# Kernel tuning notes

Hardware: AMD Instinct MI355X
Metric: run time of the kernel (lower is better)

## Reference

```python
import jax, jax.numpy as jnp
import numpy as np

B, S, D, H = 2, 2048, 1024, 16
DK = D // H  # 64
THETA = 10000.0


def setup_inputs() -> dict:
    key = jax.random.key(0)
    ks = jax.random.split(key, 5)
    std = float(np.sqrt(2.0 / (D + D)))
    x = jax.random.normal(ks[0], (B, S, D), dtype=jnp.float32)
    q_proj = jax.random.normal(ks[1], (D, D), dtype=jnp.float32) * std
    k_proj = jax.random.normal(ks[2], (D, D), dtype=jnp.float32) * std
    v_proj = jax.random.normal(ks[3], (D, D), dtype=jnp.float32) * std
    o_proj = jax.random.normal(ks[4], (D, D), dtype=jnp.float32) * std
    token_positions = jnp.arange(S, dtype=jnp.int32).reshape(1, S)
    return {"x": x, "token_positions": token_positions,
            "q_proj": q_proj, "k_proj": k_proj, "v_proj": v_proj, "o_proj": o_proj}


def _rope(t, pos):
    # t: [B, H, S, DK]; pos: [S]. Equivalent to multiplying by the block-diagonal
    # rotation matrix R[pos] in the source (interleaved 2x2 rotations).
    inv_freq = 1.0 / (THETA ** (2.0 * jnp.arange(DK // 2, dtype=jnp.float32) / DK))
    ang = pos.astype(jnp.float32)[:, None] * inv_freq[None, :]  # [S, DK/2]
    c, s = jnp.cos(ang), jnp.sin(ang)
    t0, t1 = t[..., 0::2], t[..., 1::2]
    out0 = c * t0 - s * t1
    out1 = s * t0 + c * t1
    return jnp.stack([out0, out1], axis=-1).reshape(t.shape)


def reference(x, token_positions, q_proj, k_proj, v_proj, o_proj):
    def split_heads(t):  # [B,S,D] -> [B,H,S,DK]
        return t.reshape(B, S, H, DK).transpose(0, 2, 1, 3)

    q = split_heads(jnp.einsum('bsd,ed->bse', x, q_proj))
    k = split_heads(jnp.einsum('bsd,ed->bse', x, k_proj))
    v = split_heads(jnp.einsum('bsd,ed->bse', x, v_proj))

    pos = token_positions[0]
    q = _rope(q, pos)
    k = _rope(k, pos)

    scores = jnp.einsum('bhqd,bhkd->bhqk', q, k) / jnp.sqrt(jnp.float32(DK))
    causal = jnp.tril(jnp.ones((S, S), dtype=bool))
    scores = jnp.where(causal, scores, -jnp.inf)

    # Faithful to source softmax: subtract the GLOBAL max (x.max()), then row-normalize.
    p = jnp.exp(scores - jnp.max(scores))
    p = p / jnp.sum(p, axis=-1, keepdims=True)

    attn = jnp.einsum('bhqk,bhkd->bhqd', p, v)
    attn = attn.transpose(0, 2, 1, 3).reshape(B, S, D)  # merge heads
    return jnp.einsum('bsd,ed->bse', attn, o_proj)
```

## Files before the change

### kernel.cpp

```cpp
#include <hip/hip_runtime.h>
#include <math.h>

#define B_  2
#define S_  2048
#define D_  1024
#define H_  16
#define DK_ 64
#define M_  (B_ * S_)

using u16 = unsigned short;
using u32 = unsigned int;
typedef __attribute__((ext_vector_type(8))) short  short8;
typedef __attribute__((ext_vector_type(4))) short  short4v;
typedef __attribute__((ext_vector_type(4))) float  float4v;
typedef __attribute__((ext_vector_type(4))) float  f32x4;
typedef __attribute__((ext_vector_type(4))) u32    u32x4;

__device__ __forceinline__ float bf2f(u16 h) {
  u32 u = ((u32)h) << 16;
  return __builtin_bit_cast(float, u);
}
__device__ __forceinline__ u16 f2bf(float f) {
  u32 u = __builtin_bit_cast(u32, f);
  u32 r = u + 0x7fffu + ((u >> 16) & 1u);
  return (u16)(r >> 16);
}

__device__ __forceinline__ void async16(const void* g, void* l) {
  __builtin_amdgcn_global_load_lds((const __attribute__((address_space(1))) void*)g,
                                   (__attribute__((address_space(3))) void*)l,
                                   16, 0, 0);
}

#define MFMA16(a, b, c) __builtin_amdgcn_mfma_f32_16x16x32_bf16((a), (b), (c), 0, 0, 0)

__device__ __forceinline__ void stc(u16* p, float v)   { *p = f2bf(v); }
__device__ __forceinline__ void stc(float* p, float v) { *p = v; }

#define XG_ (M_ * D_ / 4)
#define WG_ (D_ * D_ / 4)
__global__ __launch_bounds__(256) void cvt5_kernel(
    const float* __restrict__ x,  const float* __restrict__ wq,
    const float* __restrict__ wk, const float* __restrict__ wv,
    const float* __restrict__ wo, u16* __restrict__ Xb, u16* __restrict__ Wqb,
    u16* __restrict__ Wkb, u16* __restrict__ Wvb, u16* __restrict__ Wob) {
  int i = blockIdx.x * 256 + threadIdx.x;
  const float* s; u16* d; int off;
  if (i < XG_)                { s = x;  d = Xb;  off = i; }
  else if (i < XG_ + WG_)     { s = wq; d = Wqb; off = i - XG_; }
  else if (i < XG_ + 2 * WG_) { s = wk; d = Wkb; off = i - XG_ - WG_; }
  else if (i < XG_ + 3 * WG_) { s = wv; d = Wvb; off = i - XG_ - 2 * WG_; }
  else                        { s = wo; d = Wob; off = i - XG_ - 3 * WG_; }
  f32x4 v = ((const f32x4*)s)[off];
  short4v o;
  o[0] = (short)f2bf(v[0]); o[1] = (short)f2bf(v[1]);
  o[2] = (short)f2bf(v[2]); o[3] = (short)f2bf(v[3]);
  ((short4v*)d)[off] = o;
}

template <typename TC>
__device__ __forceinline__ void gemm_tile(const u16* __restrict__ A,
                                          const u16* __restrict__ Bw,
                                          TC* __restrict__ C,
                                          int K, int N, int m0, int n0) {
  __shared__ __align__(16) u16 As[128 * 32];
  __shared__ __align__(16) u16 Bs[128 * 32];
  const int tid  = threadIdx.x;
  const int lane = tid & 63;
  const int wave = tid >> 6;
  const int quad = lane >> 4;
  const int l15  = lane & 15;
  const int wm   = (wave >> 1) << 6;
  const int wn   = (wave & 1) << 6;

  float4v acc[4][4];
#pragma unroll
  for (int i = 0; i < 4; ++i)
#pragma unroll
    for (int j = 0; j < 4; ++j) acc[i][j] = (float4v){0.f, 0.f, 0.f, 0.f};

  for (int k0 = 0; k0 < K; k0 += 32) {
#pragma unroll
    for (int i = 0; i < 2; ++i) {
      const int cbase = i * 256 + wave * 64;
      const int c     = cbase + lane;
      async16(A  + (size_t)(m0 + (c >> 2)) * K + k0 + ((c & 3) << 3), As + cbase * 8);
      async16(Bw + (size_t)(n0 + (c >> 2)) * K + k0 + ((c & 3) << 3), Bs + cbase * 8);
    }
    __syncthreads();

    short8 af[4], bfr[4];
#pragma unroll
    for (int mi = 0; mi < 4; ++mi)
      af[mi] = *(const short8*)(As + (wm + mi * 16 + l15) * 32 + quad * 8);
#pragma unroll
    for (int ni = 0; ni < 4; ++ni)
      bfr[ni] = *(const short8*)(Bs + (wn + ni * 16 + l15) * 32 + quad * 8);
#pragma unroll
    for (int mi = 0; mi < 4; ++mi)
#pragma unroll
      for (int ni = 0; ni < 4; ++ni)
        acc[mi][ni] = MFMA16(af[mi], bfr[ni], acc[mi][ni]);
    __syncthreads();
  }

#pragma unroll
  for (int mi = 0; mi < 4; ++mi)
#pragma unroll
    for (int ni = 0; ni < 4; ++ni)
#pragma unroll
      for (int r = 0; r < 4; ++r) {
        const int row = m0 + wm + mi * 16 + quad * 4 + r;
        const int col = n0 + wn + ni * 16 + l15;
        stc(C + (size_t)row * N + col, acc[mi][ni][r]);
      }
}

__global__ __launch_bounds__(256) void gemm_qkv_kernel(
    const u16* __restrict__ X, const u16* __restrict__ Wq,
    const u16* __restrict__ Wk, const u16* __restrict__ Wv,
    u16* Qb, u16* Kb, u16* Vb) {
  const int mt  = blockIdx.x;
  const int nn  = blockIdx.y;
  const int sel = nn >> 3;
  const int nt  = nn & 7;
  const u16* Bw = (sel == 0) ? Wq : (sel == 1) ? Wk : Wv;
  u16*       C  = (sel == 0) ? Qb : (sel == 1) ? Kb : Vb;
  gemm_tile(X, Bw, C, D_, D_, mt * 128, nt * 128);
}

__global__ __launch_bounds__(256) void gemm_o_kernel(
    const u16* __restrict__ Ab, const u16* __restrict__ Wo, float* Out) {
  gemm_tile(Ab, Wo, Out, D_, D_, blockIdx.x * 128, blockIdx.y * 128);
}

__global__ __launch_bounds__(256) void rv_kernel(u16* __restrict__ Qb,
                                                 u16* __restrict__ Kb,
                                                 const void* __restrict__ posv,
                                                 const u16* __restrict__ Vb,
                                                 u16* __restrict__ Vt) {
  __shared__ float tabc[2][32], tabs[2][32];
  __shared__ __align__(16) u16 T[64 * 72];
  const int tid = threadIdx.x;

  if (blockIdx.x < 2048) {
    const int bx = blockIdx.x;
    const int t  = bx * 256 + tid;
    const int p4 = t & 7;
    const int h  = (t >> 3) & (H_ - 1);
    const int s  = (t >> 7) & (S_ - 1);
    const int b  = t >> 18;
    const int* p32 = (const int*)posv;
    const bool is64 = (p32[1] == 0 && p32[2] == 1);
    if (tid < 64) {
      const int sl = tid >> 5, i = tid & 31;
      const int sg = ((bx * 2) & (S_ - 1)) + sl;
      const int ps = is64 ? p32[2 * sg] : p32[sg];
      const float freq = exp2f(-0.4152410118609203f * (float)i);
      float sn, cs;
      sincosf((float)ps * freq, &sn, &cs);
      tabc[sl][i] = cs; tabs[sl][i] = sn;
    }
    __syncthreads();
    const int sl = (tid >> 7) & 1;
    const size_t base = (size_t)(b * S_ + s) * D_ + h * DK_ + p4 * 8;
    short8 qv = *(const short8*)(Qb + base);
    short8 kv = *(const short8*)(Kb + base);
    short8 qo, ko;
#pragma unroll
    for (int j = 0; j < 4; ++j) {
      const int i = p4 * 4 + j;
      const float cs = tabc[sl][i], sn = tabs[sl][i];
      const float q0v = bf2f((u16)qv[2 * j]), q1v = bf2f((u16)qv[2 * j + 1]);
      qo[2 * j]     = (short)f2bf(0.125f * (cs * q0v - sn * q1v));
      qo[2 * j + 1] = (short)f2bf(0.125f * (sn * q0v + cs * q1v));
      const float k0v = bf2f((u16)kv[2 * j]), k1v = bf2f((u16)kv[2 * j + 1]);
      ko[2 * j]     = (short)f2bf(cs * k0v - sn * k1v);
      ko[2 * j + 1] = (short)f2bf(sn * k0v + cs * k1v);
    }
    *(short8*)(Qb + base) = qo;
    *(short8*)(Kb + base) = ko;
  } else {
    const int idx  = blockIdx.x - 2048;
    const int sblk = idx & 31;
    const int bh   = idx >> 5;
    const int b = bh >> 4, h = bh & 15;
    const int s0 = sblk * 64;
    {
      const int srow = tid >> 2;
      const int dseg = (tid & 3) << 4;
      const u16* g = Vb + (size_t)(b * S_ + s0 + srow) * D_ + h * DK_ + dseg;
      *(short8*)(T + srow * 72 + dseg)     = *(const short8*)(g);
      *(short8*)(T + srow * 72 + dseg + 8) = *(const short8*)(g + 8);
    }
    __syncthreads();
    {
      const int dk   = tid >> 2;
      const int sseg = (tid & 3) << 4;
      short8 o0, o1;
#pragma unroll
      for (int jj = 0; jj < 8; ++jj) {
        const int ss0 = sseg + jj;
        const int ss1 = sseg + 8 + jj;
        const int k0l = (((ss0 & 31) >> 3) << 2) + (((ss0 >> 2) & 1) << 4) +
                        (ss0 & 3) + (ss0 & 32);
        const int k1l = (((ss1 & 31) >> 3) << 2) + (((ss1 >> 2) & 1) << 4) +
                        (ss1 & 3) + (ss1 & 32);
        o0[jj] = (short)T[k0l * 72 + dk];
        o1[jj] = (short)T[k1l * 72 + dk];
      }
      u16* g = Vt + (size_t)(bh * DK_ + dk) * S_ + s0 + sseg;
      *(short8*)(g)     = o0;
      *(short8*)(g + 8) = o1;
    }
  }
}

__global__ __launch_bounds__(256, 4) void attn_kernel(const u16* __restrict__ Qb,
                                                      const u16* __restrict__ Kb,
                                                      const u16* __restrict__ Vt,
                                                      u16* __restrict__ Ob) {
  const int j5 = (blockIdx.x + blockIdx.y) & 31;
  const int r5 = j5 & 7, g5 = j5 >> 3;
  const int qt = (g5 == 0) ? r5 : (g5 == 1) ? r5 + 8 : (g5 == 2) ? 23 - r5 : 31 - r5;
  const int bh = blockIdx.y;
  const int b = bh >> 4, h = bh & 15;
  const int tid = threadIdx.x, lane = tid & 63, wave = tid >> 6;
  const int qh = wave >> 1, kh = wave & 1;
  const int quad = lane >> 4, l15 = lane & 15;
  const int qw = qt * 64 + qh * 32;

  __shared__ __align__(16) u16 SM[2][2][64 * 64];

  const char* kp = (const char*)(Kb + (size_t)b * S_ * D_ + h * DK_);
  const char* vp = (const char*)(Vt + (size_t)bh * DK_ * S_);

  int koffb[2], voffb[2];
#pragma unroll
  for (int i = 0; i < 2; ++i) {
    const int c  = wave * 128 + i * 64 + lane;
    const int kr = c >> 3;
    const int kj = (c & 7) ^ (kr & 7);
    koffb[i] = kr * (D_ * 2) + kj * 16;
    const int vdk = c >> 3;
    const int vj  = (c & 7) ^ (vdk & 7);
    voffb[i] = vdk * (S_ * 2) + vj * 16;
  }

  auto stage = [&](int sel) {
#pragma unroll
    for (int i = 0; i < 2; ++i) {
      const int cb = wave * 128 + i * 64;
      async16(kp + koffb[i], &SM[0][sel][cb * 8]);
      async16(vp + voffb[i], &SM[1][sel][cb * 8]);
    }
    kp += 64 * D_ * 2;
    vp += 128;
  };

  const int x7   = l15 & 7;
  const int krd0 = (kh * 32 + l15) * 64 + ((quad ^ x7) << 3);
  const int krd1 = (kh * 32 + l15) * 64 + (((quad + 4) ^ x7) << 3);
  const int vrd  = l15 * 64 + (((kh * 4 + quad) ^ x7) << 3);

  short8 qf[2][2];
#pragma unroll
  for (int rg = 0; rg < 2; ++rg) {
    const u16* qrow = Qb + (size_t)(b * S_ + qw + rg * 16 + l15) * D_ + h * DK_;
    qf[rg][0] = *(const short8*)(qrow + quad * 8);
    qf[rg][1] = *(const short8*)(qrow + 32 + quad * 8);
  }

  short8 ones;
#pragma unroll
  for (int j = 0; j < 8; ++j) ones[j] = (short)0x3F80;

  float4v oacc[2][4];
#pragma unroll
  for (int rg = 0; rg < 2; ++rg)
#pragma unroll
    for (int n2 = 0; n2 < 4; ++n2) oacc[rg][n2] = (float4v){0.f, 0.f, 0.f, 0.f};
  float4v lacc[2] = {(float4v){0.f, 0.f, 0.f, 0.f}, (float4v){0.f, 0.f, 0.f, 0.f}};

  const int NS = qt + 1;
  stage(0);

  for (int j = 0; j < NS; ++j) {
    asm volatile("s_waitcnt vmcnt(0)" ::: "memory");
    __builtin_amdgcn_s_barrier();
    asm volatile("" ::: "memory");
    if (j + 1 < NS) stage((j + 1) & 1);

    const u16* ks = &SM[0][j & 1][0];
    const u16* vs = &SM[1][j & 1][0];

    float4v sc[2][2];
    __builtin_amdgcn_s_setprio(1);
#pragma unroll
    for (int ni = 0; ni < 2; ++ni) {
      const short8 kf0 = *(const short8*)(ks + krd0 + ni * 1024);
      const short8 kf1 = *(const short8*)(ks + krd1 + ni * 1024);
      float4v z = (float4v){0.f, 0.f, 0.f, 0.f};
      sc[0][ni] = MFMA16(kf1, qf[0][1], MFMA16(kf0, qf[0][0], z));
      sc[1][ni] = MFMA16(kf1, qf[1][1], MFMA16(kf0, qf[1][0], z));
    }
    __builtin_amdgcn_s_setprio(0);

    const int kb = j * 64 + kh * 32;
    if (kb + 31 > qw) {
#pragma unroll
      for (int rg = 0; rg < 2; ++rg) {
        const int qr = qw + rg * 16 + l15;
#pragma unroll
        for (int ni = 0; ni < 2; ++ni)
#pragma unroll
          for (int r = 0; r < 4; ++r) {
            const float e = __expf(sc[rg][ni][r]);
            sc[rg][ni][r] = (kb + ni * 16 + quad * 4 + r > qr) ? 0.f : e;
          }
      }
    } else {
#pragma unroll
      for (int rg = 0; rg < 2; ++rg)
#pragma unroll
        for (int ni = 0; ni < 2; ++ni)
#pragma unroll
          for (int r = 0; r < 4; ++r) sc[rg][ni][r] = __expf(sc[rg][ni][r]);
    }

    short8 pfr[2];
#pragma unroll
    for (int rg = 0; rg < 2; ++rg) {
      u32 w0, w1, w2, w3;
      asm("v_cvt_pk_bf16_f32 %0, %1, %2" : "=v"(w0) : "v"(sc[rg][0][0]), "v"(sc[rg][0][1]));
      asm("v_cvt_pk_bf16_f32 %0, %1, %2" : "=v"(w1) : "v"(sc[rg][0][2]), "v"(sc[rg][0][3]));
      asm("v_cvt_pk_bf16_f32 %0, %1, %2" : "=v"(w2) : "v"(sc[rg][1][0]), "v"(sc[rg][1][1]));
      asm("v_cvt_pk_bf16_f32 %0, %1, %2" : "=v"(w3) : "v"(sc[rg][1][2]), "v"(sc[rg][1][3]));
      u32x4 ww = (u32x4){w0, w1, w2, w3};
      pfr[rg] = __builtin_bit_cast(short8, ww);
    }

    __builtin_amdgcn_s_setprio(1);
    lacc[0] = MFMA16(pfr[0], ones, lacc[0]);
    lacc[1] = MFMA16(pfr[1], ones, lacc[1]);
#pragma unroll
    for (int n2 = 0; n2 < 4; ++n2) {
      const short8 vf = *(const short8*)(vs + vrd + n2 * 1024);
      oacc[0][n2] = MFMA16(pfr[0], vf, oacc[0][n2]);
      oacc[1][n2] = MFMA16(pfr[1], vf, oacc[1][n2]);
    }
    __builtin_amdgcn_s_setprio(0);
  }

  __syncthreads();
  float* comb = (float*)(void*)&SM[0][0][0];
  if (kh == 1) {
    float* cw = comb + (size_t)(qh * 64 + lane) * 41;
#pragma unroll
    for (int rg = 0; rg < 2; ++rg) {
#pragma unroll
      for (int n2 = 0; n2 < 4; ++n2)
#pragma unroll
        for (int r = 0; r < 4; ++r) cw[rg * 16 + n2 * 4 + r] = oacc[rg][n2][r];
#pragma unroll
      for (int r = 0; r < 4; ++r) cw[32 + rg * 4 + r] = lacc[rg][r];
    }
  }
  __syncthreads();
  if (kh == 0) {
    const float* cw = comb + (size_t)(qh * 64 + lane) * 41;
#pragma unroll
    for (int rg = 0; rg < 2; ++rg) {
      float rinv[4];
#pragma unroll
      for (int r = 0; r < 4; ++r)
        rinv[r] = 1.0f / (lacc[rg][r] + cw[32 + rg * 4 + r]);
#pragma unroll
      for (int n2 = 0; n2 < 4; ++n2)
#pragma unroll
        for (int r = 0; r < 4; ++r) {
          const int srow = qw + rg * 16 + quad * 4 + r;
          Ob[(size_t)(b * S_ + srow) * D_ + h * DK_ + n2 * 16 + l15] =
              f2bf((oacc[rg][n2][r] + cw[rg * 16 + n2 * 4 + r]) * rinv[r]);
        }
    }
  }
}

extern "C" void kernel_launch(void* const* d_in, const int* in_sizes, int n_in,
                              void* d_out, int out_size, void* d_ws, size_t ws_size,
                              hipStream_t stream) {
  const float* x  = (const float*)d_in[0];
  const void*  tp = d_in[1];
  const float* wq = (const float*)d_in[2];
  const float* wk = (const float*)d_in[3];
  const float* wv = (const float*)d_in[4];
  const float* wo = (const float*)d_in[5];
  float* out = (float*)d_out;

  u16* Qb  = (u16*)d_ws;
  u16* Kb  = Qb + (size_t)M_ * D_;
  u16* Vb  = Kb + (size_t)M_ * D_;
  u16* Vt  = Vb + (size_t)M_ * D_;
  u16* Ab  = Vt + (size_t)M_ * D_;
  u16* Xb  = Ab;
  u16* Wqb = Ab + (size_t)M_ * D_;
  u16* Wkb = Wqb + (size_t)D_ * D_;
  u16* Wvb = Wkb + (size_t)D_ * D_;
  u16* Wob = Wvb + (size_t)D_ * D_;

  cvt5_kernel<<<dim3((XG_ + 4 * WG_) / 256), dim3(256), 0, stream>>>(
      x, wq, wk, wv, wo, Xb, Wqb, Wkb, Wvb, Wob);
  gemm_qkv_kernel<<<dim3(32, 24), dim3(256), 0, stream>>>(Xb, Wqb, Wkb, Wvb, Qb, Kb, Vb);
  rv_kernel<<<dim3(3072), dim3(256), 0, stream>>>(Qb, Kb, tp, Vb, Vt);
  attn_kernel<<<dim3(32, 32), dim3(256), 0, stream>>>(Qb, Kb, Vt, Ab);
  gemm_o_kernel<<<dim3(32, 8), dim3(256), 0, stream>>>(Ab, Wob, out);
}
```

Before: 181.7 us.

## Fuse Q RoPE into attention and retile output projection to 64-row blocks

Rotary embedding and the 1/sqrt(dk) scaling for Q are now computed inside the attention kernel on the register-resident Q fragments, so rv_kernel no longer reads and writes Q through global memory. Separately, the output projection GEMM gets its own 64x128 tile kernel, launched on a 64x8 grid, to double the block count and improve occupancy across CUs. Q rotation now recomputes sincos per attention block, and the smaller tile lowers data reuse per block.

Result: no change. 178.4 us (-1.8%).

```diff
diff --git a/kernel.cpp b/kernel.cpp
--- a/kernel.cpp
+++ b/kernel.cpp
@@ -131,11 +131,63 @@
 
 __global__ __launch_bounds__(256) void gemm_o_kernel(
     const u16* __restrict__ Ab, const u16* __restrict__ Wo, float* Out) {
-  gemm_tile(Ab, Wo, Out, D_, D_, blockIdx.x * 128, blockIdx.y * 128);
-}
-
-__global__ __launch_bounds__(256) void rv_kernel(u16* __restrict__ Qb,
-                                                 u16* __restrict__ Kb,
+  __shared__ __align__(16) u16 As[64 * 32];
+  __shared__ __align__(16) u16 Bs[128 * 32];
+  const int K = D_, N = D_;
+  const int m0 = blockIdx.x * 64, n0 = blockIdx.y * 128;
+  const int tid  = threadIdx.x;
+  const int lane = tid & 63;
+  const int wave = tid >> 6;
+  const int quad = lane >> 4;
+  const int l15  = lane & 15;
+  const int wm   = (wave >> 1) << 5;
+  const int wn   = (wave & 1) << 6;
+
+  float4v acc[2][4];
+#pragma unroll
+  for (int i = 0; i < 2; ++i)
+#pragma unroll
+    for (int j = 0; j < 4; ++j) acc[i][j] = (float4v){0.f, 0.f, 0.f, 0.f};
+
+  for (int k0 = 0; k0 < K; k0 += 32) {
+    async16(Ab + (size_t)(m0 + (tid >> 2)) * K + k0 + ((tid & 3) << 3),
+            As + (wave * 64) * 8);
+#pragma unroll
+    for (int i = 0; i < 2; ++i) {
+      const int cbase = i * 256 + wave * 64;
+      const int c     = cbase + lane;
+      async16(Wo + (size_t)(n0 + (c >> 2)) * K + k0 + ((c & 3) << 3), Bs + cbase * 8);
+    }
+    __syncthreads();
+
+    short8 af[2], bfr[4];
+#pragma unroll
+    for (int mi = 0; mi < 2; ++mi)
+      af[mi] = *(const short8*)(As + (wm + mi * 16 + l15) * 32 + quad * 8);
+#pragma unroll
+    for (int ni = 0; ni < 4; ++ni)
+      bfr[ni] = *(const short8*)(Bs + (wn + ni * 16 + l15) * 32 + quad * 8);
+#pragma unroll
+    for (int mi = 0; mi < 2; ++mi)
+#pragma unroll
+      for (int ni = 0; ni < 4; ++ni)
+        acc[mi][ni] = MFMA16(af[mi], bfr[ni], acc[mi][ni]);
+    __syncthreads();
+  }
+
+#pragma unroll
+  for (int mi = 0; mi < 2; ++mi)
+#pragma unroll
+    for (int ni = 0; ni < 4; ++ni)
+#pragma unroll
+      for (int r = 0; r < 4; ++r) {
+        const int row = m0 + wm + mi * 16 + quad * 4 + r;
+        const int col = n0 + wn + ni * 16 + l15;
+        Out[(size_t)row * N + col] = acc[mi][ni][r];
+      }
+}
+
+__global__ __launch_bounds__(256) void rv_kernel(u16* __restrict__ Kb,
                                                  const void* __restrict__ posv,
                                                  const u16* __restrict__ Vb,
                                                  u16* __restrict__ Vt) {
@@ -164,21 +216,16 @@
     __syncthreads();
     const int sl = (tid >> 7) & 1;
     const size_t base = (size_t)(b * S_ + s) * D_ + h * DK_ + p4 * 8;
-    short8 qv = *(const short8*)(Qb + base);
     short8 kv = *(const short8*)(Kb + base);
-    short8 qo, ko;
+    short8 ko;
 #pragma unroll
     for (int j = 0; j < 4; ++j) {
       const int i = p4 * 4 + j;
       const float cs = tabc[sl][i], sn = tabs[sl][i];
-      const float q0v = bf2f((u16)qv[2 * j]), q1v = bf2f((u16)qv[2 * j + 1]);
-      qo[2 * j]     = (short)f2bf(0.125f * (cs * q0v - sn * q1v));
-      qo[2 * j + 1] = (short)f2bf(0.125f * (sn * q0v + cs * q1v));
       const float k0v = bf2f((u16)kv[2 * j]), k1v = bf2f((u16)kv[2 * j + 1]);
       ko[2 * j]     = (short)f2bf(cs * k0v - sn * k1v);
       ko[2 * j + 1] = (short)f2bf(sn * k0v + cs * k1v);
     }
-    *(short8*)(Qb + base) = qo;
     *(short8*)(Kb + base) = ko;
   } else {
     const int idx  = blockIdx.x - 2048;
@@ -219,7 +266,8 @@
 __global__ __launch_bounds__(256, 4) void attn_kernel(const u16* __restrict__ Qb,
                                                       const u16* __restrict__ Kb,
                                                       const u16* __restrict__ Vt,
-                                                      u16* __restrict__ Ob) {
+                                                      u16* __restrict__ Ob,
+                                                      const void* __restrict__ posv) {
   const int j5 = (blockIdx.x + blockIdx.y) & 31;
   const int r5 = j5 & 7, g5 = j5 >> 3;
   const int qt = (g5 == 0) ? r5 : (g5 == 1) ? r5 + 8 : (g5 == 2) ? 23 - r5 : 31 - r5;
@@ -269,6 +317,32 @@
     const u16* qrow = Qb + (size_t)(b * S_ + qw + rg * 16 + l15) * D_ + h * DK_;
     qf[rg][0] = *(const short8*)(qrow + quad * 8);
     qf[rg][1] = *(const short8*)(qrow + 32 + quad * 8);
+  }
+  {
+    const int* p32 = (const int*)posv;
+    const bool is64 = (p32[1] == 0 && p32[2] == 1);
+#pragma unroll
+    for (int rg = 0; rg < 2; ++rg) {
+      const int s  = qw + rg * 16 + l15;
+      const int ps = is64 ? p32[2 * s] : p32[s];
+      const float p = (float)ps;
+#pragma unroll
+      for (int pp = 0; pp < 2; ++pp) {
+        short8 q = qf[rg][pp];
+        short8 o;
+#pragma unroll
+        for (int m = 0; m < 4; ++m) {
+          const int i = pp * 16 + quad * 4 + m;
+          const float freq = exp2f(-0.4152410118609203f * (float)i);
+          float sn, cs;
+          sincosf(p * freq, &sn, &cs);
+          const float q0 = bf2f((u16)q[2 * m]), q1 = bf2f((u16)q[2 * m + 1]);
+          o[2 * m]     = (short)f2bf(0.125f * (cs * q0 - sn * q1));
+          o[2 * m + 1] = (short)f2bf(0.125f * (sn * q0 + cs * q1));
+        }
+        qf[rg][pp] = o;
+      }
+    }
   }
 
   short8 ones;
@@ -412,7 +486,7 @@
   cvt5_kernel<<<dim3((XG_ + 4 * WG_) / 256), dim3(256), 0, stream>>>(
       x, wq, wk, wv, wo, Xb, Wqb, Wkb, Wvb, Wob);
   gemm_qkv_kernel<<<dim3(32, 24), dim3(256), 0, stream>>>(Xb, Wqb, Wkb, Wvb, Qb, Kb, Vb);
-  rv_kernel<<<dim3(3072), dim3(256), 0, stream>>>(Qb, Kb, tp, Vb, Vt);
-  attn_kernel<<<dim3(32, 32), dim3(256), 0, stream>>>(Qb, Kb, Vt, Ab);
-  gemm_o_kernel<<<dim3(32, 8), dim3(256), 0, stream>>>(Ab, Wob, out);
-}
+  rv_kernel<<<dim3(3072), dim3(256), 0, stream>>>(Kb, tp, Vb, Vt);
+  attn_kernel<<<dim3(32, 32), dim3(256), 0, stream>>>(Qb, Kb, Vt, Ab, tp);
+  gemm_o_kernel<<<dim3(64, 8), dim3(256), 0, stream>>>(Ab, Wob, out);
+}
```
